# Kernel tuning notes

Measured on AMD Instinct MI355X. Metric: run time of the kernel, lower is better.

## Reference

```python
import jax, jax.numpy as jnp
import numpy as np

N_HEADS = 4
N_HIDDEN = 256  # out_features with concat=False
SLOPE = 0.1
NEG_INF = -9e15


def setup_inputs() -> dict:
    key = jax.random.key(0)
    k1, k2, k3, k4 = jax.random.split(key, 4)
    N, F_IN = 4096, 512
    h = jax.random.normal(k1, (N, F_IN), dtype=jnp.float32)
    adj_mat = jax.random.randint(k2, (N, N), 0, 2, dtype=jnp.int32)
    # xavier_normal gain=1.414
    W = jax.random.normal(k3, (F_IN, N_HIDDEN * N_HEADS), dtype=jnp.float32) * (
        1.414 * np.sqrt(2.0 / (F_IN + N_HIDDEN * N_HEADS)))
    a = jax.random.normal(k4, (N_HEADS, 2 * N_HIDDEN, 1), dtype=jnp.float32) * (
        1.414 * np.sqrt(2.0 / (2 * N_HIDDEN + 1)))
    return {"h": h, "adj_mat": adj_mat, "W": W, "a": a}


def reference(h, adj_mat, W, a):
    N = h.shape[0]
    # [N, H*D] -> [H, N, D]
    ht = (h @ W).reshape(N, N_HEADS, N_HIDDEN).transpose(1, 0, 2)
    lr = jax.nn.leaky_relu(ht, SLOPE)
    # additive attention: a split into source/target halves
    src = jnp.einsum('hnd,hd->hn', lr, a[:, :N_HIDDEN, 0])   # [H, N]
    tgt = jnp.einsum('hnd,hd->hn', lr, a[:, N_HIDDEN:, 0])   # [H, N]
    e = src[:, :, None] + tgt[:, None, :]                    # [H, N, N]
    e = jnp.where(adj_mat > 0, e, NEG_INF)
    attn = jax.nn.softmax(e, axis=-1)
    out = jnp.einsum('hnm,hmd->hnd', attn, ht)               # [H, N, D]
    return out.mean(axis=0)                                  # concat=False -> mean over heads
```

## Files before the change

### kernel.cpp

```cpp
#include <hip/hip_runtime.h>

#define N_NODES 4096
#define F_IN 512
#define NHID 256
#define HD 1024
#define NPAD 1152

typedef _Float16 half8 __attribute__((ext_vector_type(8)));
typedef _Float16 half4 __attribute__((ext_vector_type(4)));
typedef float floatx4 __attribute__((ext_vector_type(4)));
typedef float float4v __attribute__((ext_vector_type(4)));
typedef int int4v __attribute__((ext_vector_type(4)));
typedef unsigned int uint4v __attribute__((ext_vector_type(4)));

__device__ __forceinline__ float bf2f(unsigned short u) {
  union { unsigned int i; float f; } x; x.i = ((unsigned int)u) << 16; return x.f;
}

__device__ __forceinline__ void async_copy16(const void* g, void* l) {
  __builtin_amdgcn_global_load_lds((const __attribute__((address_space(1))) void*)g,
                                   (__attribute__((address_space(3))) void*)l, 16, 0, 0);
}

__global__ void detect_kernel(const unsigned short* __restrict__ hbits, int* __restrict__ flag) {
  const int t = threadIdx.x;
  int cnt = 0;
  for (int i = t; i < 1024; i += 256) {
    int e = (hbits[i] >> 7) & 0xFF;
    cnt += (e >= 115 && e <= 135) ? 1 : 0;
  }
  __shared__ int red[256];
  red[t] = cnt; __syncthreads();
  for (int s = 128; s > 0; s >>= 1) { if (t < s) red[t] += red[t + s]; __syncthreads(); }
  if (t == 0) flag[0] = (red[0] >= 900) ? 1 : 0;
}

template <typename OutT>
__device__ __forceinline__ void gemm_core(
    const _Float16* __restrict__ A, const _Float16* __restrict__ BT,
    OutT* __restrict__ C, int K, int ldc, int klen, long csz,
    int lin, int nbx, int nby, int total,
    _Float16* __restrict__ sA, _Float16* __restrict__ sB)
{
  int tile = ((total & 7) == 0) ? ((lin & 7) * (total >> 3) + (lin >> 3)) : lin;
  const int n_idx = tile % nbx;
  const int rem   = tile / nbx;
  const int m_idx = rem % nby;
  const int kz    = rem / nby;

  const int n0 = n_idx * 128;
  const int m0 = m_idx * 256;
  const int kbeg = kz * klen;
  OutT* Cz = C + (long)kz * csz;

  const int t = threadIdx.x;
  const int w = t >> 6;
  const int lane = t & 63;
  const int wm = (w >> 1) << 6;
  const int wn = (w & 1) << 6;

  floatx4 acc[4][4] = {};

  const _Float16* gA = A + (long)m0 * K;
  const _Float16* gBT = BT + (long)n0 * K;

  const int koff = (lane >> 4) << 3;
  const int rA = wm + (lane & 15);
  const int rB = wn + (lane & 15);

  const int nt = klen >> 5;

  const int rowA0 = t >> 2, koA = (t & 3) << 3;
  const int rowA1 = (512 + t) >> 2, koA1 = (t & 3) << 3;
  const int rowB = t >> 2, koB = (t & 3) << 3;

  auto STAGE = [&](int buf, int k0) {
    async_copy16(gA + (long)rowA0 * K + k0 + koA,  &sA[buf * 8192 + t * 8]);
    async_copy16(gA + (long)rowA1 * K + k0 + koA1, &sA[buf * 8192 + 4096 + t * 8]);
    async_copy16(gBT + (long)rowB * K + k0 + koB,  &sB[buf * 4096 + t * 8]);
  };

  STAGE(0, kbeg);
  if (nt > 1) STAGE(1, kbeg + 32);

  int cur = 0;
  for (int it = 0; it < nt; ++it) {
    const int k0 = kbeg + it * 32;

    if (it + 1 < nt) asm volatile("s_waitcnt vmcnt(3)" ::: "memory");
    else             asm volatile("s_waitcnt vmcnt(0)" ::: "memory");
    __builtin_amdgcn_s_barrier();

    half8 af[4], bf[4];
#pragma unroll
    for (int i = 0; i < 4; ++i)
      af[i] = *(const half8*)&sA[cur * 8192 + (rA + i * 16) * 32 + koff];
#pragma unroll
    for (int i = 0; i < 4; ++i)
      bf[i] = *(const half8*)&sB[cur * 4096 + (rB + i * 16) * 32 + koff];

    asm volatile("s_waitcnt lgkmcnt(0)" ::: "memory");
    __builtin_amdgcn_sched_barrier(0);

    const int nxt = (cur + 2 >= 3) ? cur - 1 : cur + 2;
    if (it + 2 < nt) STAGE(nxt, k0 + 64);

#pragma unroll
    for (int i = 0; i < 4; ++i)
#pragma unroll
      for (int j = 0; j < 4; ++j)
        acc[i][j] = __builtin_amdgcn_mfma_f32_16x16x32_f16(af[i], bf[j], acc[i][j], 0, 0, 0);

    cur = (cur + 1 >= 3) ? 0 : cur + 1;
  }

  const int q4 = (lane >> 4) << 2;
#pragma unroll
  for (int i = 0; i < 4; ++i) {
#pragma unroll
    for (int j = 0; j < 4; ++j) {
      const int gr = m0 + wm + i * 16 + q4;
      const int gc = n0 + wn + j * 16 + (lane & 15);
#pragma unroll
      for (int r = 0; r < 4; ++r)
        Cz[(long)(gr + r) * ldc + gc] = (OutT)acc[i][j][r];
    }
  }
}

template <typename OutT>
__global__ __launch_bounds__(512) void gemm_bt(
    const _Float16* __restrict__ A, const _Float16* __restrict__ BT,
    OutT* __restrict__ C, int K, int ldc, int klen, long csz)
{
  __shared__ _Float16 sA[3 * 256 * 32];
  __shared__ _Float16 sB[3 * 128 * 32];
  const int nbx = gridDim.x, nby = gridDim.y;
  const int total = nbx * nby * gridDim.z;
  const int lin = blockIdx.x + nbx * (blockIdx.y + nby * blockIdx.z);
  gemm_core<OutT>(A, BT, C, K, ldc, klen, csz, lin, nbx, nby, total, sA, sB);
}

__global__ __launch_bounds__(512) void fused_ht_cvt_kernel(
    const _Float16* __restrict__ hF, const _Float16* __restrict__ WT,
    _Float16* __restrict__ ht, const int* __restrict__ adj,
    _Float16* __restrict__ adjF)
{
  __shared__ _Float16 sA[3 * 256 * 32];
  __shared__ _Float16 sB[3 * 128 * 32];
  const int b = blockIdx.x;
  if (b < 128) {
    gemm_core<_Float16>(hF, WT, ht, F_IN, HD, F_IN, 0, b, 8, 16, 128, sA, sB);
  } else {
    const int i = (b - 128) * 512 + threadIdx.x;
    int4v A = ((const int4v*)adj)[2 * i];
    int4v B = ((const int4v*)adj)[2 * i + 1];
    half8 o;
#pragma unroll
    for (int e = 0; e < 4; ++e) {
      o[e]     = (_Float16)(A[e] > 0 ? 1.0f : 0.0f);
      o[4 + e] = (_Float16)(B[e] > 0 ? 1.0f : 0.0f);
    }
    ((half8*)adjF)[i] = o;
  }
}

__global__ void cvt_h_kernel(const void* __restrict__ in, _Float16* __restrict__ out,
                             const int* __restrict__ flag, int n8) {
  int i = blockIdx.x * 256 + threadIdx.x;
  if (i >= n8) return;
  half8 o;
  if (*flag) {
    union { uint4v v; unsigned short s[8]; } u;
    u.v = ((const uint4v*)in)[i];
#pragma unroll
    for (int e = 0; e < 8; ++e) o[e] = (_Float16)bf2f(u.s[e]);
  } else {
    const float4v* f = (const float4v*)in + 2 * i;
    float4v x0 = f[0], x1 = f[1];
#pragma unroll
    for (int e = 0; e < 4; ++e) { o[e] = (_Float16)x0[e]; o[4 + e] = (_Float16)x1[e]; }
  }
  ((half8*)out)[i] = o;
}

__global__ void cvt_a_kernel(const void* __restrict__ a, float* __restrict__ aF,
                             const int* __restrict__ flag) {
  const int t = threadIdx.x;
  const int bf = *flag;
#pragma unroll
  for (int e = 0; e < 8; ++e) {
    int idx = t * 8 + e;
    aF[idx] = bf ? bf2f(((const unsigned short*)a)[idx]) : ((const float*)a)[idx];
  }
}

__global__ void transpose_w_kernel(const void* __restrict__ W, _Float16* __restrict__ WT,
                                   const int* __restrict__ flag) {
  __shared__ _Float16 tile[64][72];
  const int k0 = blockIdx.x * 64, n0 = blockIdx.y * 64;
  const int t = threadIdx.x, r = t >> 3, c = t & 7;
  const int bf = *flag;
#pragma unroll
  for (int q = 0; q < 2; ++q) {
    int k = r + q * 32;
    half8 v;
    if (bf) {
      union { uint4v vv; unsigned short s[8]; } u;
      u.vv = *(const uint4v*)&((const unsigned short*)W)[(long)(k0 + k) * HD + n0 + c * 8];
#pragma unroll
      for (int e = 0; e < 8; ++e) v[e] = (_Float16)bf2f(u.s[e]);
    } else {
      const float4v* f = (const float4v*)&((const float*)W)[(long)(k0 + k) * HD + n0 + c * 8];
      float4v x0 = f[0], x1 = f[1];
#pragma unroll
      for (int e = 0; e < 4; ++e) { v[e] = (_Float16)x0[e]; v[4 + e] = (_Float16)x1[e]; }
    }
    *(half8*)&tile[k][c * 8] = v;
  }
  __syncthreads();
#pragma unroll
  for (int q = 0; q < 2; ++q) {
    int n = r + q * 32;
    half8 o;
#pragma unroll
    for (int e = 0; e < 8; ++e) o[e] = tile[c * 8 + e][n];
    *(half8*)&WT[(long)(n0 + n) * F_IN + k0 + c * 8] = o;
  }
}

__global__ void tgt_kernel(const _Float16* __restrict__ ht, const float* __restrict__ aF,
                           float* __restrict__ tgt) {
  const int i = blockIdx.x;
  const int t = threadIdx.x, h = t >> 6, lane = t & 63;
  half4 v = *(const half4*)&ht[(long)i * HD + h * NHID + lane * 4];
  float4v av = *(const float4v*)&aF[h * 512 + NHID + lane * 4];
  float s = 0.f;
#pragma unroll
  for (int e = 0; e < 4; ++e) {
    float x = (float)v[e];
    x = x > 0.f ? x : 0.1f * x;
    s += x * av[e];
  }
#pragma unroll
  for (int o = 32; o > 0; o >>= 1) s += __shfl_down(s, o);
  if (lane == 0) tgt[h * N_NODES + i] = s;
}

__global__ void maxexp_kernel(const float* __restrict__ tgt, float* __restrict__ wbuf,
                              _Float16* __restrict__ VT) {
  const int h = blockIdx.x, t = threadIdx.x;
  const float* row = tgt + h * N_NODES;
  float4v v[4];
  float m = -3.0e38f;
#pragma unroll
  for (int q = 0; q < 4; ++q) {
    v[q] = *(const float4v*)&row[(t + q * 256) * 4];
#pragma unroll
    for (int e = 0; e < 4; ++e) m = fmaxf(m, v[q][e]);
  }
#pragma unroll
  for (int o = 32; o > 0; o >>= 1) m = fmaxf(m, __shfl_down(m, o));
  __shared__ float red[4];
  if ((t & 63) == 0) red[t >> 6] = m;
  __syncthreads();
  m = fmaxf(fmaxf(red[0], red[1]), fmaxf(red[2], red[3]));
#pragma unroll
  for (int q = 0; q < 4; ++q) {
    const int j0 = (t + q * 256) * 4;
    float4v wv;
#pragma unroll
    for (int e = 0; e < 4; ++e) wv[e] = __expf(v[q][e] - m);
    *(float4v*)&wbuf[h * N_NODES + j0] = wv;
    half4 hv;
#pragma unroll
    for (int e = 0; e < 4; ++e) hv[e] = (_Float16)wv[e];
    *(half4*)&VT[(long)(HD + h) * N_NODES + j0] = hv;
  }
}

__global__ void scaled_transpose_kernel(const _Float16* __restrict__ ht, const float* __restrict__ wbuf,
                                        _Float16* __restrict__ VT) {
  __shared__ _Float16 tile[64][72];
  const int j0 = blockIdx.x * 64, n0 = blockIdx.y * 64;
  const int t = threadIdx.x, r = t >> 3, c = t & 7;
#pragma unroll
  for (int q = 0; q < 2; ++q) {
    int j = r + q * 32;
    *(half8*)&tile[j][c * 8] = *(const half8*)&ht[(long)(j0 + j) * HD + n0 + c * 8];
  }
  __syncthreads();
  const int h = n0 >> 8;
  const float* wrow = wbuf + h * N_NODES + j0;
#pragma unroll
  for (int q = 0; q < 2; ++q) {
    int n = r + q * 32;
    half8 o;
#pragma unroll
    for (int e = 0; e < 8; ++e) {
      int j = c * 8 + e;
      o[e] = (_Float16)(wrow[j] * (float)tile[j][n]);
    }
    *(half8*)&VT[(long)(n0 + n) * N_NODES + j0 + c * 8] = o;
  }
}

__global__ void epilogue_kernel(const float* __restrict__ S, float* __restrict__ out, int ns) {
  const int i = blockIdx.x, d = threadIdx.x;
  const long SZ = (long)N_NODES * NPAD;
  float num[4] = {0.f, 0.f, 0.f, 0.f};
  float den[4] = {0.f, 0.f, 0.f, 0.f};
  for (int z = 0; z < ns; ++z) {
    const float* row = S + z * SZ + (long)i * NPAD;
#pragma unroll
    for (int h = 0; h < 4; ++h) {
      num[h] += row[h * NHID + d];
      den[h] += row[HD + h];
    }
  }
  float r = 0.f;
#pragma unroll
  for (int h = 0; h < 4; ++h) r += num[h] / den[h];
  out[(long)i * NHID + d] = 0.25f * r;
}

extern "C" void kernel_launch(void* const* d_in, const int* in_sizes, int n_in,
                              void* d_out, int out_size, void* d_ws, size_t ws_size,
                              hipStream_t stream) {
  const void* h = nullptr; const int* adj = nullptr; const void* W = nullptr; const void* a = nullptr;
  for (int i = 0; i < n_in; ++i) {
    switch (in_sizes[i]) {
      case 2097152:  h   = d_in[i]; break;
      case 16777216: adj = (const int*)d_in[i]; break;
      case 524288:   W   = d_in[i]; break;
      case 2048:     a   = d_in[i]; break;
      default: break;
    }
  }
  float* out = (float*)d_out;

  char* ws = (char*)d_ws;
  const size_t OFF_ADJF = 0;
  const size_t OFF_VT   = 33554432;
  const size_t OFF_TGT  = OFF_VT + 9437184;
  const size_t OFF_WBUF = OFF_TGT + 65536;
  const size_t OFF_M    = OFF_WBUF + 65536;
  const size_t OFF_AF   = OFF_M + 256;
  const size_t OFF_X    = OFF_AF + 8192;
  const size_t SPART    = 18874368;

  int ns = 1;
  if      (ws_size >= OFF_X + 4 * SPART) ns = 4;
  else if (ws_size >= OFF_X + 2 * SPART) ns = 2;
  if (ws_size < OFF_X + SPART || !h || !adj || !W || !a) return;

  _Float16* adjF = (_Float16*)(ws + OFF_ADJF);
  _Float16* VT   = (_Float16*)(ws + OFF_VT);
  float*    tgt  = (float*)(ws + OFF_TGT);
  float*    wbuf = (float*)(ws + OFF_WBUF);
  int*      flag = (int*)(ws + OFF_M + 32);
  float*    aF   = (float*)(ws + OFF_AF);
  _Float16* hF = (_Float16*)(ws + OFF_X);
  _Float16* WT = (_Float16*)(ws + OFF_X + 4194304);
  _Float16* ht = (_Float16*)(ws + OFF_X + 5242880);
  float*    S  = (float*)(ws + OFF_X);

  detect_kernel<<<1, 256, 0, stream>>>((const unsigned short*)h, flag);
  cvt_h_kernel<<<1024, 256, 0, stream>>>(h, hF, flag, 262144);
  cvt_a_kernel<<<1, 256, 0, stream>>>(a, aF, flag);
  transpose_w_kernel<<<dim3(8, 16), 256, 0, stream>>>(W, WT, flag);
  fused_ht_cvt_kernel<<<4224, 512, 0, stream>>>(hF, WT, ht, adj, adjF);
  tgt_kernel<<<4096, 256, 0, stream>>>(ht, aF, tgt);
  maxexp_kernel<<<4, 256, 0, stream>>>(tgt, wbuf, VT);
  scaled_transpose_kernel<<<dim3(64, 16), 256, 0, stream>>>(ht, wbuf, VT);
  gemm_bt<float><<<dim3(9, 16, ns), 512, 0, stream>>>(adjF, VT, S, N_NODES, NPAD,
                                                      N_NODES / ns, (long)N_NODES * NPAD);
  epilogue_kernel<<<4096, 256, 0, stream>>>(S, out, ns);
}
```

Before: 203.2 us.

## Double GEMM K-tile to 64 with XOR-swizzled LDS and split staging

The shared GEMM core now processes a K-step of 64 per pipeline stage instead of 32. Each step runs two 32-wide MFMA sub-phases, and the next-tile async loads are split between them. LDS rows are XOR-swizzled to avoid bank conflicts on the wider rows, and s_setprio raises wave priority around the MFMA bursts. This halves loop iterations and barrier overhead but doubles LDS usage to about 144KB per block, which may reduce occupancy.

```diff
diff --git a/kernel.cpp b/kernel.cpp
--- a/kernel.cpp
+++ b/kernel.cpp
@@ -64,52 +64,75 @@
   const _Float16* gA = A + (long)m0 * K;
   const _Float16* gBT = BT + (long)n0 * K;
 
-  const int koff = (lane >> 4) << 3;
+  const int l7 = lane & 7, lg = lane >> 3;
+  const int sg = (l7 ^ lg) << 3;
   const int rA = wm + (lane & 15);
   const int rB = wn + (lane & 15);
-
-  const int nt = klen >> 5;
-
-  const int rowA0 = t >> 2, koA = (t & 3) << 3;
-  const int rowA1 = (512 + t) >> 2, koA1 = (t & 3) << 3;
-  const int rowB = t >> 2, koB = (t & 3) << 3;
-
-  auto STAGE = [&](int buf, int k0) {
-    async_copy16(gA + (long)rowA0 * K + k0 + koA,  &sA[buf * 8192 + t * 8]);
-    async_copy16(gA + (long)rowA1 * K + k0 + koA1, &sA[buf * 8192 + 4096 + t * 8]);
-    async_copy16(gBT + (long)rowB * K + k0 + koB,  &sB[buf * 4096 + t * 8]);
+  const int off0 = ((lane >> 4) ^ l7) << 3;
+  const int off1 = off0 ^ 32;
+
+  const int nt = klen >> 6;
+
+  auto STAGE_A = [&](int buf, int k0, int q) {
+    const int blk = q * 8 + w;
+    async_copy16(gA + (long)(blk * 8 + lg) * K + k0 + sg,
+                 &sA[buf * 16384 + blk * 512 + lane * 8]);
   };
-
-  STAGE(0, kbeg);
-  if (nt > 1) STAGE(1, kbeg + 32);
+  auto STAGE_B = [&](int buf, int k0, int q) {
+    const int blk = q * 8 + w;
+    async_copy16(gBT + (long)(blk * 8 + lg) * K + k0 + sg,
+                 &sB[buf * 8192 + blk * 512 + lane * 8]);
+  };
+  auto STAGE_ALL = [&](int buf, int k0) {
+    STAGE_A(buf, k0, 0); STAGE_A(buf, k0, 1); STAGE_A(buf, k0, 2); STAGE_A(buf, k0, 3);
+    STAGE_B(buf, k0, 0); STAGE_B(buf, k0, 1);
+  };
+
+  STAGE_ALL(0, kbeg);
+  if (nt > 1) STAGE_ALL(1, kbeg + 64);
 
   int cur = 0;
   for (int it = 0; it < nt; ++it) {
-    const int k0 = kbeg + it * 32;
-
-    if (it + 1 < nt) asm volatile("s_waitcnt vmcnt(3)" ::: "memory");
+    const int kN = kbeg + it * 64 + 128;
+
+    if (it + 1 < nt) asm volatile("s_waitcnt vmcnt(6)" ::: "memory");
     else             asm volatile("s_waitcnt vmcnt(0)" ::: "memory");
     __builtin_amdgcn_s_barrier();
 
+    const int nxt = (cur + 2 >= 3) ? cur - 1 : cur + 2;
+    const int aB = cur * 16384, bB = cur * 8192;
+
     half8 af[4], bf[4];
 #pragma unroll
-    for (int i = 0; i < 4; ++i)
-      af[i] = *(const half8*)&sA[cur * 8192 + (rA + i * 16) * 32 + koff];
-#pragma unroll
-    for (int i = 0; i < 4; ++i)
-      bf[i] = *(const half8*)&sB[cur * 4096 + (rB + i * 16) * 32 + koff];
-
+    for (int i = 0; i < 4; ++i) af[i] = *(const half8*)&sA[aB + (rA + i * 16) * 64 + off0];
+#pragma unroll
+    for (int j = 0; j < 4; ++j) bf[j] = *(const half8*)&sB[bB + (rB + j * 16) * 64 + off0];
+    if (it + 2 < nt) { STAGE_A(nxt, kN, 0); STAGE_A(nxt, kN, 1); }
     asm volatile("s_waitcnt lgkmcnt(0)" ::: "memory");
     __builtin_amdgcn_sched_barrier(0);
-
-    const int nxt = (cur + 2 >= 3) ? cur - 1 : cur + 2;
-    if (it + 2 < nt) STAGE(nxt, k0 + 64);
-
+    __builtin_amdgcn_s_setprio(1);
 #pragma unroll
     for (int i = 0; i < 4; ++i)
 #pragma unroll
       for (int j = 0; j < 4; ++j)
         acc[i][j] = __builtin_amdgcn_mfma_f32_16x16x32_f16(af[i], bf[j], acc[i][j], 0, 0, 0);
+    __builtin_amdgcn_s_setprio(0);
+    __builtin_amdgcn_s_barrier();
+
+#pragma unroll
+    for (int i = 0; i < 4; ++i) af[i] = *(const half8*)&sA[aB + (rA + i * 16) * 64 + off1];
+#pragma unroll
+    for (int j = 0; j < 4; ++j) bf[j] = *(const half8*)&sB[bB + (rB + j * 16) * 64 + off1];
+    if (it + 2 < nt) { STAGE_A(nxt, kN, 2); STAGE_A(nxt, kN, 3); STAGE_B(nxt, kN, 0); STAGE_B(nxt, kN, 1); }
+    asm volatile("s_waitcnt lgkmcnt(0)" ::: "memory");
+    __builtin_amdgcn_sched_barrier(0);
+    __builtin_amdgcn_s_setprio(1);
+#pragma unroll
+    for (int i = 0; i < 4; ++i)
+#pragma unroll
+      for (int j = 0; j < 4; ++j)
+        acc[i][j] = __builtin_amdgcn_mfma_f32_16x16x32_f16(af[i], bf[j], acc[i][j], 0, 0, 0);
+    __builtin_amdgcn_s_setprio(0);
 
     cur = (cur + 1 >= 3) ? 0 : cur + 1;
   }
@@ -133,8 +156,8 @@
     const _Float16* __restrict__ A, const _Float16* __restrict__ BT,
     OutT* __restrict__ C, int K, int ldc, int klen, long csz)
 {
-  __shared__ _Float16 sA[3 * 256 * 32];
-  __shared__ _Float16 sB[3 * 128 * 32];
+  __shared__ _Float16 sA[3 * 256 * 64];
+  __shared__ _Float16 sB[3 * 128 * 64];
   const int nbx = gridDim.x, nby = gridDim.y;
   const int total = nbx * nby * gridDim.z;
   const int lin = blockIdx.x + nbx * (blockIdx.y + nby * blockIdx.z);
@@ -146,8 +169,8 @@
     _Float16* __restrict__ ht, const int* __restrict__ adj,
     _Float16* __restrict__ adjF)
 {
-  __shared__ _Float16 sA[3 * 256 * 32];
-  __shared__ _Float16 sB[3 * 128 * 32];
+  __shared__ _Float16 sA[3 * 256 * 64];
+  __shared__ _Float16 sB[3 * 128 * 64];
   const int b = blockIdx.x;
   if (b < 128) {
     gemm_core<_Float16>(hF, WT, ht, F_IN, HD, F_IN, 0, b, 8, 16, 128, sA, sB);
```

Result: no change. 203.1 us (-0.0%).
